# Optimization experiments

Measured on AMD Instinct MI355X. Metric: run time of the kernel, lower is better.

Reference implementation:

```python
import jax, jax.numpy as jnp
import numpy as np

N, K, D, H = 16384, 8, 128, 256  # nodes, preds per node, emb dim, hidden


def _build_graph():
    i = np.arange(1, N + 1)[:, None]      # [N,1] node ids 1..N
    k = np.arange(K)[None, :]             # [1,K]
    pred = i - 1 - k                       # predecessor node ids
    mask = pred >= 0
    pred_nodes = np.maximum(pred, 0).astype(np.int32)        # [N,K]
    end = np.repeat(np.arange(1, N + 1), K).astype(np.int32)  # [N*K]
    edges = np.stack([pred_nodes.reshape(-1), end], axis=1)   # [E,2]
    pred_edge_idx = (np.arange(N * K).reshape(N, K) + 1).astype(np.int32)  # +1: zero row prepended to distances
    return pred_nodes, pred_edge_idx, mask, edges.astype(np.int32)


def setup_inputs() -> dict:
    key = jax.random.key(0)
    k1, k2, k3 = jax.random.split(key, 3)
    pred_nodes, pred_edge_idx, mask, edges = _build_graph()
    s1 = 1.0 / np.sqrt(2 * D)
    s2 = 1.0 / np.sqrt(H)
    return {
        "words_embs": jax.random.normal(k1, (N + 1, D), dtype=jnp.float32),
        "W1": jax.random.uniform(k2, (2 * D, H), jnp.float32, -s1, s1),
        "b1": jnp.zeros((H,), jnp.float32),
        "W2": jax.random.uniform(k3, (H, 1), jnp.float32, -s2, s2),
        "b2": jnp.zeros((1,), jnp.float32),
        "best_idxs": jnp.arange(N + 1, dtype=jnp.int32),  # the chain path 0->1->...->N
        "edges": jnp.asarray(edges),
        "pred_nodes": jnp.asarray(pred_nodes),
        "pred_edge_idx": jnp.asarray(pred_edge_idx),
        "pred_mask": jnp.asarray(mask),
    }


def _distance(x, y, W1, b1, W2, b2):
    # MLP over concatenated pair features: Linear -> Tanh -> Linear -> Softplus
    h = jnp.tanh(jnp.concatenate([x, y], axis=-1) @ W1 + b1)
    return jax.nn.softplus(h @ W2 + b2)  # [...,1]


def _forward_alg(words_embs, edges, pred_nodes, pred_edge_idx, pred_mask, W1, b1, W2, b2):
    n_nodes = pred_nodes.shape[0]
    d = _distance(words_embs[edges[:, 0]], words_embs[edges[:, 1]], W1, b1, W2, b2)  # [E,1]
    dists = jnp.concatenate([jnp.zeros((1, 1), d.dtype), d], axis=0)[:, 0]  # [E+1]
    esum0 = jnp.zeros((n_nodes + 1,), d.dtype)
    neg_inf = jnp.asarray(-jnp.inf, d.dtype)

    def step(esum, inp):
        i, preds, eidx, m = inp
        vals = jnp.where(m, esum[preds] - dists[eidx], neg_inf)  # [K]
        mx = jnp.max(vals)
        lse = mx + jnp.log(jnp.sum(jnp.exp(vals - mx)))
        return esum.at[i].set(lse), None

    idxs = jnp.arange(1, n_nodes + 1, dtype=jnp.int32)
    esum, _ = jax.lax.scan(step, esum0, (idxs, pred_nodes, pred_edge_idx, pred_mask))
    return esum[-1]


def reference(words_embs, W1, b1, W2, b2, best_idxs, edges, pred_nodes, pred_edge_idx, pred_mask):
    # gold path score
    feats = words_embs[best_idxs]  # [P,D]
    gold = _distance(feats[:-1], feats[1:], W1, b1, W2, b2).sum(0)  # [1]
    # partition-function-like forward score over the lattice
    fwd = _forward_alg(words_embs, edges, pred_nodes, pred_edge_idx, pred_mask, W1, b1, W2, b2)
    return (gold + fwd).mean()  # single-sample version of loss_fuc
```

## Files before the change

kernel.cpp:

```cpp
#include <hip/hip_runtime.h>
#include <math.h>

#define NV 16385
#define NEDGE 131072
#define NEG -1e30f
#define SCALE 2.8853900817779268f

typedef __attribute__((ext_vector_type(8))) short short8;
typedef __attribute__((ext_vector_type(4))) float f32x4;

__device__ float g_part[4 * NEDGE];
__device__ float g_mats[32 * 64];
__device__ float g_gold;
__device__ unsigned short g_embh[16408 * 128];
__device__ unsigned short g_w1bf[8192 * 8];

__device__ __forceinline__ unsigned short f2bf(float x) {
  union { float f; unsigned int u; } c; c.f = x;
  unsigned int u = c.u;
  unsigned int r = (u + 0x7fffu + ((u >> 16) & 1u)) >> 16;
  return (unsigned short)r;
}

__device__ __forceinline__ void gll16(const void* g, void* l) {
  __builtin_amdgcn_global_load_lds(
      (const __attribute__((address_space(1))) unsigned int*)g,
      (__attribute__((address_space(3))) unsigned int*)l, 16, 0, 0);
}

__device__ __forceinline__ float lse8(float x0, float x1, float x2, float x3,
                                      float x4, float x5, float x6, float x7) {
  float m = fmaxf(fmaxf(fmaxf(x0, x1), fmaxf(x2, x3)),
                  fmaxf(fmaxf(x4, x5), fmaxf(x6, x7)));
  float s = __expf(x0 - m) + __expf(x1 - m) + __expf(x2 - m) + __expf(x3 - m) +
            __expf(x4 - m) + __expf(x5 - m) + __expf(x6 - m) + __expf(x7 - m);
  return m + __logf(s);
}

__device__ __forceinline__ float comb8(float A, float B, int i8, int j) {
  float x0 = __shfl(A, i8 + 0) + __shfl(B, 0 + j);
  float x1 = __shfl(A, i8 + 1) + __shfl(B, 8 + j);
  float x2 = __shfl(A, i8 + 2) + __shfl(B, 16 + j);
  float x3 = __shfl(A, i8 + 3) + __shfl(B, 24 + j);
  float x4 = __shfl(A, i8 + 4) + __shfl(B, 32 + j);
  float x5 = __shfl(A, i8 + 5) + __shfl(B, 40 + j);
  float x6 = __shfl(A, i8 + 6) + __shfl(B, 48 + j);
  float x7 = __shfl(A, i8 + 7) + __shfl(B, 56 + j);
  return lse8(x0, x1, x2, x3, x4, x5, x6, x7);
}

#define ETERM(ea, eb, w, acc)                              \
  {                                                        \
    float e_ = (ea) * (eb);                                \
    acc = fmaf(__builtin_amdgcn_rcpf(e_ + 1.f), (w), acc); \
  }

__global__ __launch_bounds__(256) void k_prep(const float* __restrict__ emb,
                                              const float* __restrict__ W1) {
  const int gid = blockIdx.x * 256 + threadIdx.x;
  for (int i = gid; i < 16408 * 16; i += 256 * 256) {
    const int r = i >> 4, g = i & 15;
    const int key = (r - 1) & 7;
    const int v = r - 8;
    uint4 o = make_uint4(0u, 0u, 0u, 0u);
    if (v >= 0 && v < NV) {
      const float* src = &emb[v * 128 + ((g ^ key) << 3)];
      float4 a = *(const float4*)src;
      float4 b = *(const float4*)(src + 4);
      o.x = f2bf(a.x) | ((unsigned int)f2bf(a.y) << 16);
      o.y = f2bf(a.z) | ((unsigned int)f2bf(a.w) << 16);
      o.z = f2bf(b.x) | ((unsigned int)f2bf(b.y) << 16);
      o.w = f2bf(b.z) | ((unsigned int)f2bf(b.w) << 16);
    }
    *(uint4*)&g_embh[(r << 7) + (g << 3)] = o;
  }
  if (gid < 8192) {
    const int tt = gid & 255;
    const int fh = gid >> 8;
    const int hx = fh & 3, f = fh >> 2;
    const int wv = tt >> 6, lane = tt & 63;
    const int l15 = lane & 15, quad = lane >> 4;
    const int col = (hx << 6) + (wv << 4) + l15;
    const int kb = ((f & 3) << 5) + (quad << 3) + ((f >> 2) << 7);
    unsigned int w[4];
#pragma unroll
    for (int i = 0; i < 8; i += 2) {
      float a0 = W1[(kb + i) * 256 + col];
      float a1 = W1[(kb + i + 1) * 256 + col];
      w[i >> 1] = f2bf(a0) | ((unsigned int)f2bf(a1) << 16);
    }
    *(uint4*)&g_w1bf[gid << 3] = *(const uint4*)w;
  }
}

__global__ __launch_bounds__(256, 4) void k12_fused(const float* __restrict__ b1,
                                                    const float* __restrict__ W2) {
  __shared__ __align__(16) unsigned short lds[19088];
  unsigned short* Es = lds;
  float* CA = (float*)lds;
  float* CB = (float*)(lds + 10240);
  float* W2s = (float*)(lds + 18944);
  float* Wsum = (float*)(lds + 19072);

  const int t = threadIdx.x;
  const int hx = blockIdx.x;
  const int h0 = hx << 6;
  const int i0 = (int)blockIdx.y << 6;
  const int wv = t >> 6, lane = t & 63;
  const int l15 = lane & 15, quad = lane >> 4;

  {
    const char* src = (const char*)&g_embh[(i0 + 1) << 7];
    char* dst = (char*)lds;
#pragma unroll
    for (int p = 0; p < 5; ++p) {
      const int off = (p << 12) + (wv << 10);
      gll16(src + off + (lane << 4), dst + off);
    }
  }

  if (t < 64) W2s[t] = -2.f * W2[h0 + t];
  if (t < 8) {
    float s = 0.f;
#pragma unroll
    for (int jj = 0; jj < 8; ++jj) s += W2[h0 + (t << 3) + jj];
    Wsum[t] = s;
  }

  short8 fA[4], fB[4];
#pragma unroll
  for (int kc = 0; kc < 4; ++kc) {
    fA[kc] = *(const short8*)&g_w1bf[((((kc << 2) + hx) << 8) + t) << 3];
    fB[kc] = *(const short8*)&g_w1bf[((((16 + (kc << 2)) + hx) << 8) + t) << 3];
  }

  f32x4 accA[5], accB[4];
#pragma unroll
  for (int m = 0; m < 5; ++m) accA[m] = (f32x4){0.f, 0.f, 0.f, 0.f};
#pragma unroll
  for (int m = 0; m < 4; ++m) accB[m] = (f32x4){0.f, 0.f, 0.f, 0.f};

  __syncthreads();

#pragma unroll
  for (int kc = 0; kc < 4; ++kc) {
    const int cb = (kc << 5) + (quad << 3);
#pragma unroll
    for (int mf = 0; mf < 5; ++mf) {
      const int row = (mf << 4) + l15;
      short8 a = *(const short8*)&Es[(row << 7) + (cb ^ ((row & 7) << 3))];
      accA[mf] = __builtin_amdgcn_mfma_f32_16x16x32_bf16(a, fA[kc], accA[mf], 0, 0, 0);
    }
#pragma unroll
    for (int mf = 0; mf < 4; ++mf) {
      const int row = 8 + (mf << 4) + l15;
      short8 a = *(const short8*)&Es[(row << 7) + (cb ^ ((row & 7) << 3))];
      accB[mf] = __builtin_amdgcn_mfma_f32_16x16x32_bf16(a, fB[kc], accB[mf], 0, 0, 0);
    }
  }
  __syncthreads();
  const int hcol = (wv << 4) + l15;
  const float b1s = b1[h0 + hcol];
#pragma unroll
  for (int mf = 0; mf < 5; ++mf) {
    int rb = (mf << 4) + (quad << 2);
#pragma unroll
    for (int rr = 0; rr < 4; ++rr)
      if (rb + rr < 71)
        CA[(rb + rr) * 68 + hcol] =
            __builtin_amdgcn_exp2f((accA[mf][rr] + b1s) * SCALE);
  }
#pragma unroll
  for (int mf = 0; mf < 4; ++mf) {
    int rb = (mf << 4) + (quad << 2);
#pragma unroll
    for (int rr = 0; rr < 4; ++rr)
      CB[(rb + rr) * 68 + hcol] = __builtin_amdgcn_exp2f(accB[mf][rr] * SCALE);
  }
  __syncthreads();
  const int k = t & 7;
  const int qb = t >> 3;
  float ws_all = 0.f;
#pragma unroll
  for (int s = 0; s < 8; ++s) ws_all += Wsum[s];
  float pa0 = 0.f, pa1 = 0.f, pb0 = 0.f, pb1 = 0.f;
#pragma unroll
  for (int g = 0; g < 8; ++g) {
    const int s = (g + (k << 1)) & 7;
    const float* wp = &W2s[s << 3];
    float4 w0 = *(const float4*)wp;
    float4 w1 = *(const float4*)(wp + 4);
    {
      const float* ap = &CA[(7 + qb - k) * 68 + (s << 3)];
      const float* bp = &CB[qb * 68 + (s << 3)];
      float4 a0 = *(const float4*)ap, a1 = *(const float4*)(ap + 4);
      float4 b0 = *(const float4*)bp, b1v = *(const float4*)(bp + 4);
      ETERM(a0.x, b0.x, w0.x, pa0); ETERM(a0.y, b0.y, w0.y, pa0);
      ETERM(a0.z, b0.z, w0.z, pa0); ETERM(a0.w, b0.w, w0.w, pa0);
      ETERM(a1.x, b1v.x, w1.x, pa1); ETERM(a1.y, b1v.y, w1.y, pa1);
      ETERM(a1.z, b1v.z, w1.z, pa1); ETERM(a1.w, b1v.w, w1.w, pa1);
    }
    {
      const int q = qb + 32;
      const float* ap = &CA[(7 + q - k) * 68 + (s << 3)];
      const float* bp = &CB[q * 68 + (s << 3)];
      float4 a0 = *(const float4*)ap, a1 = *(const float4*)(ap + 4);
      float4 b0 = *(const float4*)bp, b1v = *(const float4*)(bp + 4);
      ETERM(a0.x, b0.x, w0.x, pb0); ETERM(a0.y, b0.y, w0.y, pb0);
      ETERM(a0.z, b0.z, w0.z, pb0); ETERM(a0.w, b0.w, w0.w, pb0);
      ETERM(a1.x, b1v.x, w1.x, pb1); ETERM(a1.y, b1v.y, w1.y, pb1);
      ETERM(a1.z, b1v.z, w1.z, pb1); ETERM(a1.w, b1v.w, w1.w, pb1);
    }
  }
  const int ebase = hx * NEDGE + ((int)blockIdx.y << 9) + t;
  g_part[ebase] = (pa0 + pa1) + ws_all;
  g_part[ebase + 256] = (pb0 + pb1) + ws_all;
}

__global__ __launch_bounds__(256) void k_tail1(const float* __restrict__ b2) {
  __shared__ float wf[64][64];
  __shared__ float m8[8][64];
  const int t = threadIdx.x;
  const int b = blockIdx.x;
  const float b2v = b2[0];
  float gold = 0.f;
#pragma unroll
  for (int it = 0; it < 4; ++it) {
    const int e4 = t + (it << 8);
    const int gidx = (b << 10) + e4;
    float4 s0 = *(const float4*)&g_part[gidx << 2];
    float4 s1 = *(const float4*)&g_part[NEDGE + (gidx << 2)];
    float4 s2 = *(const float4*)&g_part[2 * NEDGE + (gidx << 2)];
    float4 s3 = *(const float4*)&g_part[3 * NEDGE + (gidx << 2)];
    float d0 = s0.x + s1.x + s2.x + s3.x + b2v;
    float d1 = s0.y + s1.y + s2.y + s3.y + b2v;
    float d2 = s0.z + s1.z + s2.z + s3.z + b2v;
    float d3 = s0.w + s1.w + s2.w + s3.w + b2v;
    d0 = fmaxf(d0, 0.f) + log1pf(__expf(-fabsf(d0)));
    d1 = fmaxf(d1, 0.f) + log1pf(__expf(-fabsf(d1)));
    d2 = fmaxf(d2, 0.f) + log1pf(__expf(-fabsf(d2)));
    d3 = fmaxf(d3, 0.f) + log1pf(__expf(-fabsf(d3)));
    const int q = e4 << 2;
    const int cl = q >> 9, r = q & 511;
    const int s = r >> 3, kk = r & 7;
    *(float4*)&wf[s][(cl << 3) + kk] = make_float4(d0, d1, d2, d3);
    if ((t & 1) == 0) gold += d0;
  }
#pragma unroll
  for (int off = 32; off > 0; off >>= 1) gold += __shfl_xor(gold, off, 64);
  if ((t & 63) == 0) atomicAdd(&g_gold, gold);
  __syncthreads();
  if (b == 0 && t == 0) {
    for (int s = 0; s < 7; ++s)
      for (int kk = s + 1; kk < 8; ++kk) wf[s][kk] = 1e30f;
  }
  __syncthreads();
  if (t < 64) {
    const int g = t >> 3, j = t & 7;
    float P[8];
#pragma unroll
    for (int kk = 0; kk < 8; ++kk) P[kk] = (kk == j) ? 0.f : NEG;
    for (int s = 0; s < 64; ++s) {
      const float* wp = &wf[s][g << 3];
      float4 wa = *(const float4*)wp;
      float4 wb = *(const float4*)(wp + 4);
      float nv = lse8(P[0] - wa.x, P[1] - wa.y, P[2] - wa.z, P[3] - wa.w,
                      P[4] - wb.x, P[5] - wb.y, P[6] - wb.z, P[7] - wb.w);
#pragma unroll
      for (int kk = 7; kk > 0; --kk) P[kk] = P[kk - 1];
      P[0] = nv;
    }
#pragma unroll
    for (int kk = 0; kk < 8; ++kk) m8[g][(kk << 3) + j] = P[kk];
    const int i8 = (t >> 3) << 3;
    float R = m8[0][t];
#pragma unroll
    for (int g2 = 1; g2 < 8; ++g2) R = comb8(m8[g2][t], R, i8, j);
    g_mats[(b << 6) + t] = R;
  }
}

__global__ __launch_bounds__(256) void k_tail2(float* __restrict__ out) {
  __shared__ float l2m[4][64];
  const int t = threadIdx.x;
  const int l = t & 63, w = t >> 6;
  const int i8 = (l >> 3) << 3, j = l & 7;
  float G = g_mats[((w << 3) << 6) + l];
#pragma unroll
  for (int s2 = 1; s2 < 8; ++s2)
    G = comb8(g_mats[(((w << 3) + s2) << 6) + l], G, i8, j);
  l2m[w][l] = G;
  __syncthreads();
  if (t < 64) {
    float G2 = l2m[0][t];
#pragma unroll
    for (int w2 = 1; w2 < 4; ++w2) G2 = comb8(l2m[w2][t], G2, i8, j);
    if (t == 0) {
      out[0] = g_gold + G2;
      g_gold = 0.f;
    }
  }
}

extern "C" void kernel_launch(void* const* d_in, const int* in_sizes, int n_in,
                              void* d_out, int out_size, void* d_ws, size_t ws_size,
                              hipStream_t stream) {
  const float* emb = (const float*)d_in[0];
  const float* W1 = (const float*)d_in[1];
  const float* b1 = (const float*)d_in[2];
  const float* W2 = (const float*)d_in[3];
  const float* b2 = (const float*)d_in[4];
  float* out = (float*)d_out;
  hipLaunchKernelGGL(k_prep, dim3(256), dim3(256), 0, stream, emb, W1);
  hipLaunchKernelGGL(k12_fused, dim3(4, 256), dim3(256), 0, stream, b1, W2);
  hipLaunchKernelGGL(k_tail1, dim3(32), dim3(256), 0, stream, b2);
  hipLaunchKernelGGL(k_tail2, dim3(1), dim3(256), 0, stream, out);
}
```

Measured before the change: 110.1 us.

## Merge tail kernels via last-block atomic counter and reorder fused grid

Fuses the two tail kernels into one by having each block bump a global counter after storing its partial matrix, with the last block doing the final reduction. This removes one kernel launch and the gap between launches. It also swaps the grid axes of the fused MLP kernel so consecutive blocks walk node tiles within one hidden slice, and changes the LDS access rotation. The risk is memory-ordering subtleties: the stores use relaxed atomics and only the reader side does an acquire, with no release fence before the counter increment.

```diff
diff --git a/kernel.cpp b/kernel.cpp
--- a/kernel.cpp
+++ b/kernel.cpp
@@ -12,6 +12,7 @@
 __device__ float g_part[4 * NEDGE];
 __device__ float g_mats[32 * 64];
 __device__ float g_gold;
+__device__ int g_done;
 __device__ unsigned short g_embh[16408 * 128];
 __device__ unsigned short g_w1bf[8192 * 8];
 
@@ -103,9 +104,9 @@
   float* Wsum = (float*)(lds + 19072);
 
   const int t = threadIdx.x;
-  const int hx = blockIdx.x;
+  const int hx = blockIdx.y;
   const int h0 = hx << 6;
-  const int i0 = (int)blockIdx.y << 6;
+  const int i0 = (int)blockIdx.x << 6;
   const int wv = t >> 6, lane = t & 63;
   const int l15 = lane & 15, quad = lane >> 4;
 
@@ -186,7 +187,7 @@
   float pa0 = 0.f, pa1 = 0.f, pb0 = 0.f, pb1 = 0.f;
 #pragma unroll
   for (int g = 0; g < 8; ++g) {
-    const int s = (g + (k << 1)) & 7;
+    const int s = (g + k) & 7;
     const float* wp = &W2s[s << 3];
     float4 w0 = *(const float4*)wp;
     float4 w1 = *(const float4*)(wp + 4);
@@ -212,14 +213,17 @@
       ETERM(a1.z, b1v.z, w1.z, pb1); ETERM(a1.w, b1v.w, w1.w, pb1);
     }
   }
-  const int ebase = hx * NEDGE + ((int)blockIdx.y << 9) + t;
+  const int ebase = hx * NEDGE + ((int)blockIdx.x << 9) + t;
   g_part[ebase] = (pa0 + pa1) + ws_all;
   g_part[ebase + 256] = (pb0 + pb1) + ws_all;
 }
 
-__global__ __launch_bounds__(256) void k_tail1(const float* __restrict__ b2) {
+__global__ __launch_bounds__(256) void k_tail(const float* __restrict__ b2,
+                                              float* __restrict__ out) {
   __shared__ float wf[64][64];
   __shared__ float m8[8][64];
+  __shared__ float l2m[4][64];
+  __shared__ int flag;
   const int t = threadIdx.x;
   const int b = blockIdx.x;
   const float b2v = b2[0];
@@ -276,28 +280,44 @@
     float R = m8[0][t];
 #pragma unroll
     for (int g2 = 1; g2 < 8; ++g2) R = comb8(m8[g2][t], R, i8, j);
-    g_mats[(b << 6) + t] = R;
-  }
-}
-
-__global__ __launch_bounds__(256) void k_tail2(float* __restrict__ out) {
-  __shared__ float l2m[4][64];
-  const int t = threadIdx.x;
-  const int l = t & 63, w = t >> 6;
-  const int i8 = (l >> 3) << 3, j = l & 7;
-  float G = g_mats[((w << 3) << 6) + l];
-#pragma unroll
-  for (int s2 = 1; s2 < 8; ++s2)
-    G = comb8(g_mats[(((w << 3) + s2) << 6) + l], G, i8, j);
-  l2m[w][l] = G;
-  __syncthreads();
-  if (t < 64) {
-    float G2 = l2m[0][t];
-#pragma unroll
-    for (int w2 = 1; w2 < 4; ++w2) G2 = comb8(l2m[w2][t], G2, i8, j);
-    if (t == 0) {
-      out[0] = g_gold + G2;
-      g_gold = 0.f;
+    __hip_atomic_store(&g_mats[(b << 6) + t], R, __ATOMIC_RELAXED,
+                       __HIP_MEMORY_SCOPE_AGENT);
+  }
+  __syncthreads();
+  if (t == 0) {
+    int old = __hip_atomic_fetch_add(&g_done, 1, __ATOMIC_RELAXED,
+                                     __HIP_MEMORY_SCOPE_AGENT);
+    flag = (old == 31);
+  }
+  __syncthreads();
+  if (!flag) return;
+
+  if (t == 0)
+    (void)__hip_atomic_load(&g_done, __ATOMIC_ACQUIRE,
+                            __HIP_MEMORY_SCOPE_AGENT);
+  __syncthreads();
+  {
+    const int l = t & 63, w = t >> 6;
+    const int i8 = (l >> 3) << 3, j = l & 7;
+    float G = g_mats[((w << 3) << 6) + l];
+#pragma unroll
+    for (int s2 = 1; s2 < 8; ++s2)
+      G = comb8(g_mats[(((w << 3) + s2) << 6) + l], G, i8, j);
+    l2m[w][l] = G;
+    __syncthreads();
+    if (t < 64) {
+      float G2 = l2m[0][t];
+#pragma unroll
+      for (int w2 = 1; w2 < 4; ++w2) G2 = comb8(l2m[w2][t], G2, i8, j);
+      if (t == 0) {
+        float gg = __hip_atomic_load(&g_gold, __ATOMIC_RELAXED,
+                                     __HIP_MEMORY_SCOPE_AGENT);
+        out[0] = gg + G2;
+        __hip_atomic_store(&g_gold, 0.f, __ATOMIC_RELAXED,
+                           __HIP_MEMORY_SCOPE_AGENT);
+        __hip_atomic_store(&g_done, 0, __ATOMIC_RELAXED,
+                           __HIP_MEMORY_SCOPE_AGENT);
+      }
     }
   }
 }
@@ -312,7 +332,6 @@
   const float* b2 = (const float*)d_in[4];
   float* out = (float*)d_out;
   hipLaunchKernelGGL(k_prep, dim3(256), dim3(256), 0, stream, emb, W1);
-  hipLaunchKernelGGL(k12_fused, dim3(4, 256), dim3(256), 0, stream, b1, W2);
-  hipLaunchKernelGGL(k_tail1, dim3(32), dim3(256), 0, stream, b2);
-  hipLaunchKernelGGL(k_tail2, dim3(1), dim3(256), 0, stream, out);
-}
+  hipLaunchKernelGGL(k12_fused, dim3(256, 4), dim3(256), 0, stream, b1, W2);
+  hipLaunchKernelGGL(k_tail, dim3(32), dim3(256), 0, stream, b2, out);
+}
```

After: 110.9 us. About the same (+0.7%).
